# Kernel tuning notes

Measured on AMD Instinct MI355X. Metric: run time of the kernel, lower is better.

The kernel has to match this reference:

```python
import jax, jax.numpy as jnp
import numpy as np
import math

H, D = 8, 128            # num_heads, head_dim (hidden=1024)
CHUNK, PAST, FUT = 12, 12, 0
CTX = CHUNK + PAST + FUT  # 24
SOFTCAP = 50.0
INVALID = 1e-09
Q_SCALE = D ** (-0.5) / math.log(2)
K_SCALE = math.log(1.0 + math.e) / math.log(2)


def setup_inputs() -> dict:
    key = jax.random.key(0)
    ks = jax.random.split(key, 7)
    B, S, HS = 16, 2400, 1024
    w = lambda k: jax.random.normal(k, (HS, HS), jnp.float32) * 0.02
    return {
        "x": jax.random.normal(ks[0], (B, S, HS), jnp.float32),
        "pos_emb": jax.random.normal(ks[1], (CTX + 1, HS), jnp.float32),
        "Wq": w(ks[2]),
        "Wk": w(ks[3]),
        "Wv": w(ks[4]),
        "Wpost": w(ks[5]),
        "Wrel": w(ks[6]),
        "per_dim_scale": jnp.zeros((D,), jnp.float32),
    }


def _to_blocks(t):
    # [B,S,H,D] -> [B,nb,CHUNK,H,D] (pad S up to multiple of CHUNK)
    B, S, h, d = t.shape
    nb = -(-S // CHUNK)
    t = jnp.pad(t, ((0, 0), (0, nb * CHUNK - S), (0, 0), (0, 0)))
    return t.reshape(B, nb, CHUNK, h, d)


def _block_context(t):
    # [B,S,H,D] -> [B,nb,CTX,H,D]: per-block window of PAST left context + chunk + FUT
    B, S, h, d = t.shape
    nb = -(-S // CHUNK)
    tp = jnp.pad(t, ((0, 0), (PAST, FUT + CHUNK - 1), (0, 0), (0, 0)))
    idx = jnp.arange(nb)[:, None] * CHUNK + jnp.arange(CTX)[None, :]  # [nb,CTX]
    return tp[:, idx]  # gather -> [B,nb,CTX,H,D]


def _rel_shift(x):
    # [B,H,nb,CHUNK,P] -> [B,H,nb,CHUNK,CTX] via Transformer-XL reshape trick
    B, h, nb, bs, P = x.shape
    x = jnp.pad(x, ((0, 0), (0, 0), (0, 0), (0, 0), (0, CTX + 1 - P)))
    x = x.reshape(B, h, nb, bs * (CTX + 1))[..., : bs * CTX]
    return x.reshape(B, h, nb, bs, CTX)


def reference(x, pos_emb, Wq, Wk, Wv, Wpost, Wrel, per_dim_scale):
    B, S, HS = x.shape
    q = (x @ Wq).reshape(B, S, H, D) * Q_SCALE * jax.nn.softplus(per_dim_scale)
    k = (x @ Wk).reshape(B, S, H, D) * K_SCALE
    v = (x @ Wv).reshape(B, S, H, D)

    qb = _to_blocks(q)        # [B,nb,CHUNK,H,D]
    kc = _block_context(k)    # [B,nb,CTX,H,D]
    vc = _block_context(v)    # [B,nb,CTX,H,D]
    nb = qb.shape[1]

    rel_k = (pos_emb @ Wrel).reshape(-1, H, D)  # [P,H,D]

    # content-content scores: [B,H,nb,CHUNK,CTX]
    matrix_ac = jnp.einsum('bnqhd,bnkhd->bhnqk', qb, kc)
    # content-position scores with rel-shift: [B,H,nb,CHUNK,P] -> [...,CTX]
    matrix_bd = jnp.einsum('bnqhd,phd->bhnqp', qb, rel_k)
    matrix_bd = _rel_shift(matrix_bd)

    attn = jnp.tanh((matrix_ac + matrix_bd) / SOFTCAP) * SOFTCAP
    attn = jax.nn.softmax(attn, axis=-1)

    out = jnp.einsum('bhnqk,bnkhd->bnqhd', attn, vc)  # [B,nb,CHUNK,H,D]
    out = out.reshape(B, nb * CHUNK, H * D)[:, :S, :]
    return out @ Wpost
```

## Files before the change

### kernel.cpp

```cpp
#include <hip/hip_runtime.h>
#include <hip/hip_bf16.h>
#include <cmath>

#define AS_GLOBAL __attribute__((address_space(1)))
#define AS_LDS    __attribute__((address_space(3)))

typedef __attribute__((ext_vector_type(8))) short bf16x8;
typedef __attribute__((ext_vector_type(4))) float f32x4;
typedef unsigned short u16;

__device__ __forceinline__ u16 f2bf(float f) {
  union { __hip_bfloat16 h; u16 u; } cv;
  cv.h = __float2bfloat16(f);
  return cv.u;
}
__device__ __forceinline__ float bf2f(u16 u) {
  union { unsigned u32; float f; } v;
  v.u32 = ((unsigned)u) << 16;
  return v.f;
}


__global__ void k_f32_to_bf16(const float* __restrict__ in, u16* __restrict__ out, int n4) {
  int i = blockIdx.x * 256 + threadIdx.x;
  if (i >= n4) return;
  float4 v = ((const float4*)in)[i];
  ushort4 o;
  o.x = f2bf(v.x); o.y = f2bf(v.y); o.z = f2bf(v.z); o.w = f2bf(v.w);
  ((ushort4*)out)[i] = o;
}

__global__ void k_transpose_w(const float* __restrict__ in, u16* __restrict__ out) {
  __shared__ float tile[32][33];
  const int tx = threadIdx.x & 31;
  const int ty = threadIdx.x >> 5;
  const int x0 = blockIdx.x * 32, y0 = blockIdx.y * 32;
  #pragma unroll
  for (int i = 0; i < 32; i += 8)
    tile[ty + i][tx] = in[(size_t)(y0 + ty + i) * 1024 + x0 + tx];
  __syncthreads();
  #pragma unroll
  for (int i = 0; i < 32; i += 8)
    out[(size_t)(x0 + ty + i) * 1024 + y0 + tx] = f2bf(tile[tx][ty + i]);
}

__global__ void k_qscale(const float* __restrict__ pds, float* __restrict__ qs, float qscale_c) {
  int n = blockIdx.x * 256 + threadIdx.x;
  float s = pds[n & 127];
  qs[n] = qscale_c * log1pf(expf(s));
}

__global__ void k_relk(const float* __restrict__ pos, const u16* __restrict__ wrt,
                       u16* __restrict__ relkb) {
  __shared__ float prow[1024];
  const int tid = threadIdx.x;
  const int p = blockIdx.y;
  ((float4*)prow)[tid] = ((const float4*)(pos + (size_t)p * 1024))[tid];
  __syncthreads();
  int nn = blockIdx.x * 256 + tid;
  const u16* wr = wrt + (size_t)nn * 1024;
  float acc = 0.f;
  for (int kk = 0; kk < 1024; kk += 8) {
    ushort4 u0 = *(const ushort4*)(wr + kk);
    ushort4 u1 = *(const ushort4*)(wr + kk + 4);
    acc += bf2f(u0.x) * prow[kk + 0] + bf2f(u0.y) * prow[kk + 1]
         + bf2f(u0.z) * prow[kk + 2] + bf2f(u0.w) * prow[kk + 3]
         + bf2f(u1.x) * prow[kk + 4] + bf2f(u1.y) * prow[kk + 5]
         + bf2f(u1.z) * prow[kk + 6] + bf2f(u1.w) * prow[kk + 7];
  }
  relkb[(size_t)p * 1024 + nn] = f2bf(acc);
}


#define VMCNT(n) do { asm volatile("s_waitcnt vmcnt(" #n ")" ::: "memory"); \
                      __builtin_amdgcn_sched_barrier(0); } while (0)
#define BARF() do { asm volatile("" ::: "memory"); __builtin_amdgcn_s_barrier(); asm volatile("" ::: "memory"); } while (0)
#define GLD(SRC, DST) __builtin_amdgcn_global_load_lds((const AS_GLOBAL u16*)(SRC), (AS_LDS u16*)(DST), 16, 0, 0)
#define LDSA(d) ((AS_LDS char*)&lds[d][0][0])
#define LDSB(d) ((AS_LDS char*)&lds[d][1][0])

#define STAGE_A(d, h, t) do {                                                   \
  GLD(sA0 + (((size_t)(h)) << 6) * K + ((t) << 6), LDSA(d) + dA0 + ((h) << 13)); \
  GLD(sA1 + (((size_t)(h)) << 6) * K + ((t) << 6), LDSA(d) + dA1 + ((h) << 13)); \
} while (0)
#define STAGE_B(d, h, t) do {                                                   \
  GLD(sB0 + (((size_t)(h)) << 5) * K + ((t) << 6), LDSB(d) + dB0 + ((h) << 12)); \
  GLD(sB1 + (((size_t)(h)) << 5) * K + ((t) << 6), LDSB(d) + dB1 + ((h) << 12)); \
} while (0)

#define LOAD_A(d, qm) do {                                                       \
  _Pragma("unroll") for (int mi_ = 0; mi_ < 4; ++mi_) {                          \
    af[mi_][0] = *(const bf16x8*)&lds[d][0][abase + (((qm)*64 + mi_*16) << 6) + gk0]; \
    af[mi_][1] = *(const bf16x8*)&lds[d][0][abase + (((qm)*64 + mi_*16) << 6) + gk1]; \
  } } while (0)
#define LOAD_B(d, qn) do {                                                       \
  _Pragma("unroll") for (int ni_ = 0; ni_ < 2; ++ni_) {                          \
    bfb[ni_][0] = *(const bf16x8*)&lds[d][1][bbase + (((qn)*32 + ni_*16) << 6) + gk0]; \
    bfb[ni_][1] = *(const bf16x8*)&lds[d][1][bbase + (((qn)*32 + ni_*16) << 6) + gk1]; \
  } } while (0)
#define MFMA16(qm, qn) do {                                                      \
  __builtin_amdgcn_s_setprio(1);                                                 \
  _Pragma("unroll") for (int mi_ = 0; mi_ < 4; ++mi_)                            \
  _Pragma("unroll") for (int ni_ = 0; ni_ < 2; ++ni_) {                          \
    acc[(qm)*4+mi_][(qn)*2+ni_] = __builtin_amdgcn_mfma_f32_16x16x32_bf16(       \
        af[mi_][0], bfb[ni_][0], acc[(qm)*4+mi_][(qn)*2+ni_], 0, 0, 0);          \
    acc[(qm)*4+mi_][(qn)*2+ni_] = __builtin_amdgcn_mfma_f32_16x16x32_bf16(       \
        af[mi_][1], bfb[ni_][1], acc[(qm)*4+mi_][(qn)*2+ni_], 0, 0, 0);          \
  }                                                                              \
  __builtin_amdgcn_s_setprio(0); } while (0)

#define GEMM_MAINLOOP()                                                          \
  STAGE_B(0, 0, 0);  STAGE_A(0, 1, 0);  STAGE_A(0, 0, 0);  STAGE_B(0, 1, 0);     \
  STAGE_B(1, 0, 1);  STAGE_A(1, 1, 1);                                           \
  VMCNT(6);  BARF();                                                             \
  const int nk = K >> 6;                                                         \
  for (int i = 0; i < (nk >> 1) - 1; ++i) {                                      \
    const int t1 = 2 * i + 1, t2 = 2 * i + 2, t3 = 2 * i + 3;                    \
    LOAD_A(0, 0); LOAD_B(0, 0);                                                  \
    STAGE_A(1, 0, t1);                                                           \
    BARF(); MFMA16(0, 0); BARF();                                                \
    LOAD_A(0, 1);                                                                \
    STAGE_B(1, 1, t1);                                                           \
    BARF(); MFMA16(1, 0); VMCNT(8); BARF();                                      \
    LOAD_B(0, 1);                                                                \
    STAGE_B(0, 0, t2);                                                           \
    BARF(); MFMA16(1, 1); BARF();                                                \
    LOAD_A(0, 0);                                                                \
    STAGE_A(0, 1, t2);                                                           \
    BARF(); MFMA16(0, 1); VMCNT(6); BARF();                                      \
    LOAD_A(1, 0); LOAD_B(1, 0);                                                  \
    STAGE_A(0, 0, t2);                                                           \
    BARF(); MFMA16(0, 0); BARF();                                                \
    LOAD_A(1, 1);                                                                \
    STAGE_B(0, 1, t2);                                                           \
    BARF(); MFMA16(1, 0); VMCNT(8); BARF();                                      \
    LOAD_B(1, 1);                                                                \
    STAGE_B(1, 0, t3);                                                           \
    BARF(); MFMA16(1, 1); BARF();                                                \
    LOAD_A(1, 0);                                                                \
    STAGE_A(1, 1, t3);                                                           \
    BARF(); MFMA16(0, 1); VMCNT(6); BARF();                                      \
  }                                                                              \
  {                                                                              \
    const int t1 = nk - 1;                                                       \
    LOAD_A(0, 0); LOAD_B(0, 0);                                                  \
    STAGE_A(1, 0, t1);                                                           \
    BARF(); MFMA16(0, 0); BARF();                                                \
    LOAD_A(0, 1);                                                                \
    STAGE_B(1, 1, t1);                                                           \
    BARF(); MFMA16(1, 0); VMCNT(8); BARF();                                      \
    LOAD_B(0, 1);                                                                \
    BARF(); MFMA16(1, 1); BARF();                                                \
    LOAD_A(0, 0);                                                                \
    BARF(); MFMA16(0, 1); VMCNT(2); BARF();                                      \
    LOAD_A(1, 0); LOAD_B(1, 0);                                                  \
    BARF(); MFMA16(0, 0); BARF();                                                \
    LOAD_A(1, 1);                                                                \
    BARF(); MFMA16(1, 0); VMCNT(0); BARF();                                      \
    LOAD_B(1, 1);                                                                \
    BARF(); MFMA16(1, 1); BARF();                                                \
    LOAD_A(1, 0);                                                                \
    BARF(); MFMA16(0, 1);                                                        \
  }

#define GEMM_SETUP(NTN)                                                          \
  __shared__ __align__(16) u16 lds[2][2][16384];                                 \
  const int tid = threadIdx.x;                                                   \
  const int wave = tid >> 6, lane = tid & 63;                                    \
  const int l16 = lane & 15, quad = lane >> 4;                                   \
  const int wm = wave >> 2, wn = wave & 3;                                       \
  const int q8 = (int)gridDim.x >> 3;                                            \
  const int wg = ((int)blockIdx.x & 7) * q8 + ((int)blockIdx.x >> 3);            \
  const int m0 = (wg / (NTN)) << 8;                                              \
  const int n0 = (wg % (NTN)) << 8;                                              \
  const int sx = l16 & 7;                                                        \
  const int gk0 = (quad ^ sx) << 3;                                              \
  const int gk1 = ((4 + quad) ^ sx) << 3;                                        \
  const int abase = (wm * 128 + l16) << 6;                                       \
  const int bbase = (wn * 64 + l16) << 6;                                        \
  const int rl0 = tid >> 3, g0 = tid & 7;                                        \
  const int rl1 = rl0 + 64;                                                      \
  const int swz0 = (g0 ^ (rl0 & 7)) << 3;                                        \
  const int rbA0 = ((rl0 >> 6) << 7) + (rl0 & 63);                               \
  const int rbA1 = ((rl1 >> 6) << 7) + (rl1 & 63);                               \
  const int rbB0 = ((rl0 >> 5) << 6) + (rl0 & 31);                               \
  const int rbB1 = ((rl1 >> 5) << 6) + (rl1 & 31);                               \
  const u16* sA0 = A + (size_t)(m0 + rbA0) * K + swz0;                           \
  const u16* sA1 = A + (size_t)(m0 + rbA1) * K + swz0;                           \
  const u16* sB0 = Bt + (size_t)(n0 + rbB0) * K + swz0;                          \
  const u16* sB1 = Bt + (size_t)(n0 + rbB1) * K + swz0;                          \
  const int dA0 = (rbA0 << 7) + (g0 << 4);                                       \
  const int dA1 = (rbA1 << 7) + (g0 << 4);                                       \
  const int dB0 = (rbB0 << 7) + (g0 << 4);                                       \
  const int dB1 = (rbB1 << 7) + (g0 << 4);                                       \
  f32x4 acc[8][4];                                                               \
  _Pragma("unroll") for (int i = 0; i < 8; ++i)                                  \
    _Pragma("unroll") for (int j = 0; j < 4; ++j) {                              \
      f32x4 z = {0.f, 0.f, 0.f, 0.f};                                            \
      acc[i][j] = z;                                                             \
    }                                                                            \
  bf16x8 af[4][2], bfb[2][2];

__global__ __launch_bounds__(512, 2) void k_gemm256(
    const u16* __restrict__ A, const u16* __restrict__ Bt, float* __restrict__ Cout,
    int M, int N, int K) {
  GEMM_SETUP(N >> 8)
  GEMM_MAINLOOP()
  const int mb = m0 + wm * 128, nb = n0 + wn * 64;
  #pragma unroll
  for (int ni = 0; ni < 4; ++ni) {
    int col = nb + ni * 16 + l16;
    #pragma unroll
    for (int mi = 0; mi < 8; ++mi) {
      int row = mb + mi * 16 + quad * 4;
      #pragma unroll
      for (int r = 0; r < 4; ++r)
        Cout[(size_t)(row + r) * N + col] = acc[mi][ni][r];
    }
  }
}

__global__ __launch_bounds__(512, 2) void k_gemm_qkv(
    const u16* __restrict__ A, const u16* __restrict__ Bt,
    u16* __restrict__ Qo, u16* __restrict__ Ko, u16* __restrict__ Vt,
    const float* __restrict__ qsc, float ks, int M, int K) {
  GEMM_SETUP(12)
  GEMM_MAINLOOP()
  const int sec = n0 >> 10;
  const int mb = m0 + wm * 128;
  const int nbl = (n0 & 1023) + wn * 64;
  if (sec == 2) {
    #pragma unroll
    for (int ni = 0; ni < 4; ++ni) {
      int col = nbl + ni * 16 + l16;
      #pragma unroll
      for (int mi = 0; mi < 8; ++mi) {
        int row = mb + mi * 16 + quad * 4;
        ushort4 o;
        o.x = f2bf(acc[mi][ni][0]);
        o.y = f2bf(acc[mi][ni][1]);
        o.z = f2bf(acc[mi][ni][2]);
        o.w = f2bf(acc[mi][ni][3]);
        *(ushort4*)&Vt[(size_t)col * M + row] = o;
      }
    }
  } else {
    u16* Out = (sec == 0) ? Qo : Ko;
    #pragma unroll
    for (int ni = 0; ni < 4; ++ni) {
      int col = nbl + ni * 16 + l16;
      float cs = (sec == 0) ? qsc[col] : ks;
      #pragma unroll
      for (int mi = 0; mi < 8; ++mi) {
        int row = mb + mi * 16 + quad * 4;
        #pragma unroll
        for (int r = 0; r < 4; ++r)
          Out[(size_t)(row + r) * 1024 + col] = f2bf(acc[mi][ni][r] * cs);
      }
    }
  }
}

#undef GEMM_SETUP
#undef GEMM_MAINLOOP
#undef STAGE_A
#undef STAGE_B
#undef LOAD_A
#undef LOAD_B
#undef MFMA16

__global__ __launch_bounds__(256) void k_attn_mfma(
    const u16* __restrict__ q, const u16* __restrict__ k, const u16* __restrict__ vt,
    const u16* __restrict__ relkb, u16* __restrict__ ctx) {
  __shared__ float bdm_s[4][400];
  __shared__ u16 attnb[4][16 * 32];

  const int tid = threadIdx.x;
  const int w = tid >> 6, lane = tid & 63;
  const int l16 = lane & 15, quad = lane >> 4;

  for (int id0 = (int)blockIdx.x * 4; id0 < 25600; id0 += (int)gridDim.x * 4) {
    const int id = id0 + w;
    const int b = id / 1600;
    const int rr = id % 1600;
    const int n = rr >> 3, h = rr & 7;
    const int s0 = n * 12;
    const size_t rowbase = (size_t)b * 2400;

    bf16x8 qf[4];
    {
      int sq = s0 + l16;
      if (sq > 2399) sq = 2399;
      const u16* qp = q + ((rowbase + sq) * 1024 + (size_t)h * 128 + quad * 8);
      #pragma unroll
      for (int c = 0; c < 4; ++c) qf[c] = *(const bf16x8*)(qp + 32 * c);
    }

    #pragma unroll
    for (int pt = 0; pt < 2; ++pt) {
      int p = pt * 16 + l16;
      const u16* rp = relkb + ((size_t)p * 1024 + (size_t)h * 128 + quad * 8);
      f32x4 acc = {0.f, 0.f, 0.f, 0.f};
      #pragma unroll
      for (int c = 0; c < 4; ++c)
        acc = __builtin_amdgcn_mfma_f32_16x16x32_bf16(qf[c], *(const bf16x8*)(rp + 32 * c), acc, 0, 0, 0);
      if (p < 25) {
        #pragma unroll
        for (int r = 0; r < 4; ++r)
          bdm_s[w][(quad * 4 + r) * 25 + p] = acc[r];
      }
    }
    __threadfence_block();

    float l0[4], l1[4];
    #pragma unroll
    for (int kt = 0; kt < 2; ++kt) {
      int t = kt * 16 + l16;
      int sk = s0 - 12 + t;
      bool kvalid = ((unsigned)sk < 2400u);
      int ska = kvalid ? sk : 0;
      const u16* kp = k + ((rowbase + ska) * 1024 + (size_t)h * 128 + quad * 8);
      short km = kvalid ? (short)0xFFFF : (short)0;
      bf16x8 kmv = {km, km, km, km, km, km, km, km};
      f32x4 acc = {0.f, 0.f, 0.f, 0.f};
      #pragma unroll
      for (int c = 0; c < 4; ++c) {
        bf16x8 kf = *(const bf16x8*)(kp + 32 * c);
        kf &= kmv;
        acc = __builtin_amdgcn_mfma_f32_16x16x32_bf16(qf[c], kf, acc, 0, 0, 0);
      }
      #pragma unroll
      for (int r = 0; r < 4; ++r) {
        float bd = bdm_s[w][(quad * 4 + r) * 24 + t];
        float lg = tanhf((acc[r] + bd) * (1.0f / 50.0f)) * 50.0f;
        if (kt == 1 && l16 >= 8) lg = -INFINITY;
        if (kt) l1[r] = lg; else l0[r] = lg;
      }
    }

    float at0[4], at1[4];
    #pragma unroll
    for (int r = 0; r < 4; ++r) {
      float m = fmaxf(l0[r], l1[r]);
      #pragma unroll
      for (int s = 1; s < 16; s <<= 1) m = fmaxf(m, __shfl_xor(m, s, 64));
      float e0 = __expf(l0[r] - m), e1 = __expf(l1[r] - m);
      float sum = e0 + e1;
      #pragma unroll
      for (int s = 1; s < 16; s <<= 1) sum += __shfl_xor(sum, s, 64);
      float inv = 1.0f / sum;
      at0[r] = e0 * inv;
      at1[r] = e1 * inv;
    }

    #pragma unroll
    for (int r = 0; r < 4; ++r) {
      attnb[w][(quad * 4 + r) * 32 + l16] = f2bf(at0[r]);
      attnb[w][(quad * 4 + r) * 32 + 16 + l16] = f2bf(at1[r]);
    }
    __threadfence_block();
    bf16x8 paf = *(const bf16x8*)&attnb[w][l16 * 32 + quad * 8];

    int slo = s0 - 12 + quad * 8;
    bf16x8 vmsk;
    #pragma unroll
    for (int j = 0; j < 8; ++j)
      vmsk[j] = ((unsigned)(slo + j) < 2400u) ? (short)0xFFFF : (short)0;

    f32x4 oacc[8];
    #pragma unroll
    for (int dt = 0; dt < 8; ++dt) {
      int col = h * 128 + dt * 16 + l16;
      const u16* vp = vt + ((size_t)col * 38400 + (long)(rowbase + s0 - 12 + quad * 8));
      ushort4 va = *(const ushort4*)vp;
      ushort4 vb = *(const ushort4*)(vp + 4);
      bf16x8 vf = {(short)va.x, (short)va.y, (short)va.z, (short)va.w,
                   (short)vb.x, (short)vb.y, (short)vb.z, (short)vb.w};
      vf &= vmsk;
      f32x4 z = {0.f, 0.f, 0.f, 0.f};
      oacc[dt] = __builtin_amdgcn_mfma_f32_16x16x32_bf16(paf, vf, z, 0, 0, 0);
    }

    if (quad < 3) {
      #pragma unroll
      for (int dt = 0; dt < 8; ++dt) {
        int col = h * 128 + dt * 16 + l16;
        #pragma unroll
        for (int r = 0; r < 4; ++r) {
          int qi = quad * 4 + r;
          ctx[(rowbase + s0 + qi) * 1024 + col] = f2bf(oacc[dt][r]);
        }
      }
    }
  }
}


extern "C" void kernel_launch(void* const* d_in, const int* in_sizes, int n_in,
                              void* d_out, int out_size, void* d_ws, size_t ws_size,
                              hipStream_t stream) {
  const float* x       = (const float*)d_in[0];
  const float* pos_emb = (const float*)d_in[1];
  const float* Wq      = (const float*)d_in[2];
  const float* Wk      = (const float*)d_in[3];
  const float* Wv      = (const float*)d_in[4];
  const float* Wpost   = (const float*)d_in[5];
  const float* Wrel    = (const float*)d_in[6];
  const float* pds     = (const float*)d_in[7];
  float* out = (float*)d_out;

  const int M = 38400, HS = 1024;
  const size_t XE = (size_t)M * HS;

  u16* xbf = (u16*)d_ws;
  u16* qbf = xbf + XE;
  u16* kbf = qbf + XE;
  u16* vt_alloc = kbf + XE;
  u16* vt = vt_alloc + 16;
  u16* wqt = vt_alloc + XE + 64;
  u16* wkt = wqt + (size_t)HS * HS;
  u16* wvt = wkt + (size_t)HS * HS;
  u16* wrt = wvt + (size_t)HS * HS;
  u16* wpt = wrt + (size_t)HS * HS;
  u16* relkb = wpt + (size_t)HS * HS;
  float* qsc = (float*)(relkb + 32 * 1024);

  const double LN2 = 0.6931471805599453;
  const float QS = (float)((1.0 / sqrt(128.0)) / LN2);
  const float KS = (float)(log(1.0 + exp(1.0)) / LN2);

  k_f32_to_bf16<<<(int)(XE / 4 / 256), 256, 0, stream>>>(x, xbf, (int)(XE / 4));
  dim3 tg(32, 32);
  k_transpose_w<<<tg, 256, 0, stream>>>(Wq, wqt);
  k_transpose_w<<<tg, 256, 0, stream>>>(Wk, wkt);
  k_transpose_w<<<tg, 256, 0, stream>>>(Wv, wvt);
  k_transpose_w<<<tg, 256, 0, stream>>>(Wrel, wrt);
  k_transpose_w<<<tg, 256, 0, stream>>>(Wpost, wpt);
  k_qscale<<<4, 256, 0, stream>>>(pds, qsc, QS);
  k_relk<<<dim3(4, 25), 256, 0, stream>>>(pos_emb, wrt, relkb);
  k_gemm_qkv<<<(M / 256) * 12, 512, 0, stream>>>(xbf, wqt, qbf, kbf, vt, qsc, KS, M, HS);
  k_attn_mfma<<<2048, 256, 0, stream>>>(qbf, kbf, vt, relkb, xbf);
  k_gemm256<<<(M / 256) * (HS / 256), 512, 0, stream>>>(xbf, wpt, out, M, HS, HS);
}
```

Baseline: 798.3 us.

## Swap MFMA operands for row-contiguous vector stores and regroup QKV GEMM tile order

New measurement: 831.6 us. +4.2%, slower.

```diff
diff --git a/kernel.cpp b/kernel.cpp
--- a/kernel.cpp
+++ b/kernel.cpp
@@ -98,7 +98,7 @@
     bfb[ni_][0] = *(const bf16x8*)&lds[d][1][bbase + (((qn)*32 + ni_*16) << 6) + gk0]; \
     bfb[ni_][1] = *(const bf16x8*)&lds[d][1][bbase + (((qn)*32 + ni_*16) << 6) + gk1]; \
   } } while (0)
-#define MFMA16(qm, qn) do {                                                      \
+#define MFMA16_N(qm, qn) do {                                                    \
   __builtin_amdgcn_s_setprio(1);                                                 \
   _Pragma("unroll") for (int mi_ = 0; mi_ < 4; ++mi_)                            \
   _Pragma("unroll") for (int ni_ = 0; ni_ < 2; ++ni_) {                          \
@@ -108,8 +108,18 @@
         af[mi_][1], bfb[ni_][1], acc[(qm)*4+mi_][(qn)*2+ni_], 0, 0, 0);          \
   }                                                                              \
   __builtin_amdgcn_s_setprio(0); } while (0)
-
-#define GEMM_MAINLOOP()                                                          \
+#define MFMA16_S(qm, qn) do {                                                    \
+  __builtin_amdgcn_s_setprio(1);                                                 \
+  _Pragma("unroll") for (int mi_ = 0; mi_ < 4; ++mi_)                            \
+  _Pragma("unroll") for (int ni_ = 0; ni_ < 2; ++ni_) {                          \
+    acc[(qm)*4+mi_][(qn)*2+ni_] = __builtin_amdgcn_mfma_f32_16x16x32_bf16(       \
+        bfb[ni_][0], af[mi_][0], acc[(qm)*4+mi_][(qn)*2+ni_], 0, 0, 0);          \
+    acc[(qm)*4+mi_][(qn)*2+ni_] = __builtin_amdgcn_mfma_f32_16x16x32_bf16(       \
+        bfb[ni_][1], af[mi_][1], acc[(qm)*4+mi_][(qn)*2+ni_], 0, 0, 0);          \
+  }                                                                              \
+  __builtin_amdgcn_s_setprio(0); } while (0)
+
+#define GEMM_MAINLOOP(MM)                                                        \
   STAGE_B(0, 0, 0);  STAGE_A(0, 1, 0);  STAGE_A(0, 0, 0);  STAGE_B(0, 1, 0);     \
   STAGE_B(1, 0, 1);  STAGE_A(1, 1, 1);                                           \
   VMCNT(6);  BARF();                                                             \
@@ -118,61 +128,52 @@
     const int t1 = 2 * i + 1, t2 = 2 * i + 2, t3 = 2 * i + 3;                    \
     LOAD_A(0, 0); LOAD_B(0, 0);                                                  \
     STAGE_A(1, 0, t1);                                                           \
-    BARF(); MFMA16(0, 0); BARF();                                                \
+    BARF(); MM(0, 0); BARF();                                                    \
     LOAD_A(0, 1);                                                                \
     STAGE_B(1, 1, t1);                                                           \
-    BARF(); MFMA16(1, 0); VMCNT(8); BARF();                                      \
+    BARF(); MM(1, 0); VMCNT(8); BARF();                                          \
     LOAD_B(0, 1);                                                                \
     STAGE_B(0, 0, t2);                                                           \
-    BARF(); MFMA16(1, 1); BARF();                                                \
+    BARF(); MM(1, 1); BARF();                                                    \
     LOAD_A(0, 0);                                                                \
     STAGE_A(0, 1, t2);                                                           \
-    BARF(); MFMA16(0, 1); VMCNT(6); BARF();                                      \
+    BARF(); MM(0, 1); VMCNT(6); BARF();                                          \
     LOAD_A(1, 0); LOAD_B(1, 0);                                                  \
     STAGE_A(0, 0, t2);                                                           \
-    BARF(); MFMA16(0, 0); BARF();                                                \
+    BARF(); MM(0, 0); BARF();                                                    \
     LOAD_A(1, 1);                                                                \
     STAGE_B(0, 1, t2);                                                           \
-    BARF(); MFMA16(1, 0); VMCNT(8); BARF();                                      \
+    BARF(); MM(1, 0); VMCNT(8); BARF();                                          \
     LOAD_B(1, 1);                                                                \
     STAGE_B(1, 0, t3);                                                           \
-    BARF(); MFMA16(1, 1); BARF();                                                \
+    BARF(); MM(1, 1); BARF();                                                    \
     LOAD_A(1, 0);                                                                \
     STAGE_A(1, 1, t3);                                                           \
-    BARF(); MFMA16(0, 1); VMCNT(6); BARF();                                      \
+    BARF(); MM(0, 1); VMCNT(6); BARF();                                          \
   }                                                                              \
   {                                                                              \
     const int t1 = nk - 1;                                                       \
     LOAD_A(0, 0); LOAD_B(0, 0);                                                  \
     STAGE_A(1, 0, t1);                                                           \
-    BARF(); MFMA16(0, 0); BARF();                                                \
+    BARF(); MM(0, 0); BARF();                                                    \
     LOAD_A(0, 1);                                                                \
     STAGE_B(1, 1, t1);                                                           \
-    BARF(); MFMA16(1, 0); VMCNT(8); BARF();                                      \
+    BARF(); MM(1, 0); VMCNT(8); BARF();                                          \
     LOAD_B(0, 1);                                                                \
-    BARF(); MFMA16(1, 1); BARF();                                                \
+    BARF(); MM(1, 1); BARF();                                                    \
     LOAD_A(0, 0);                                                                \
-    BARF(); MFMA16(0, 1); VMCNT(2); BARF();                                      \
+    BARF(); MM(0, 1); VMCNT(2); BARF();                                          \
     LOAD_A(1, 0); LOAD_B(1, 0);                                                  \
-    BARF(); MFMA16(0, 0); BARF();                                                \
+    BARF(); MM(0, 0); BARF();                                                    \
     LOAD_A(1, 1);                                                                \
-    BARF(); MFMA16(1, 0); VMCNT(0); BARF();                                      \
+    BARF(); MM(1, 0); VMCNT(0); BARF();                                          \
     LOAD_B(1, 1);                                                                \
-    BARF(); MFMA16(1, 1); BARF();                                                \
+    BARF(); MM(1, 1); BARF();                                                    \
     LOAD_A(1, 0);                                                                \
-    BARF(); MFMA16(0, 1);                                                        \
+    BARF(); MM(0, 1);                                                            \
   }
 
-#define GEMM_SETUP(NTN)                                                          \
-  __shared__ __align__(16) u16 lds[2][2][16384];                                 \
-  const int tid = threadIdx.x;                                                   \
-  const int wave = tid >> 6, lane = tid & 63;                                    \
-  const int l16 = lane & 15, quad = lane >> 4;                                   \
-  const int wm = wave >> 2, wn = wave & 3;                                       \
-  const int q8 = (int)gridDim.x >> 3;                                            \
-  const int wg = ((int)blockIdx.x & 7) * q8 + ((int)blockIdx.x >> 3);            \
-  const int m0 = (wg / (NTN)) << 8;                                              \
-  const int n0 = (wg % (NTN)) << 8;                                              \
+#define GEMM_SETUP()                                                             \
   const int sx = l16 & 7;                                                        \
   const int gk0 = (quad ^ sx) << 3;                                              \
   const int gk1 = ((4 + quad) ^ sx) << 3;                                        \
@@ -204,18 +205,26 @@
 __global__ __launch_bounds__(512, 2) void k_gemm256(
     const u16* __restrict__ A, const u16* __restrict__ Bt, float* __restrict__ Cout,
     int M, int N, int K) {
-  GEMM_SETUP(N >> 8)
-  GEMM_MAINLOOP()
+  __shared__ __align__(16) u16 lds[2][2][16384];
+  const int tid = threadIdx.x;
+  const int wave = tid >> 6, lane = tid & 63;
+  const int l16 = lane & 15, quad = lane >> 4;
+  const int wm = wave >> 2, wn = wave & 3;
+  const int q8 = (int)gridDim.x >> 3;
+  const int wg = ((int)blockIdx.x & 7) * q8 + ((int)blockIdx.x >> 3);
+  const int ntn = N >> 8;
+  const int m0 = (wg / ntn) << 8;
+  const int n0 = (wg % ntn) << 8;
+  GEMM_SETUP()
+  GEMM_MAINLOOP(MFMA16_S)
   const int mb = m0 + wm * 128, nb = n0 + wn * 64;
   #pragma unroll
   for (int ni = 0; ni < 4; ++ni) {
-    int col = nb + ni * 16 + l16;
+    int colb = nb + ni * 16 + quad * 4;
     #pragma unroll
     for (int mi = 0; mi < 8; ++mi) {
-      int row = mb + mi * 16 + quad * 4;
-      #pragma unroll
-      for (int r = 0; r < 4; ++r)
-        Cout[(size_t)(row + r) * N + col] = acc[mi][ni][r];
+      int row = mb + mi * 16 + l16;
+      *(f32x4*)&Cout[(size_t)row * N + colb] = acc[mi][ni];
     }
   }
 }
@@ -224,12 +233,22 @@
     const u16* __restrict__ A, const u16* __restrict__ Bt,
     u16* __restrict__ Qo, u16* __restrict__ Ko, u16* __restrict__ Vt,
     const float* __restrict__ qsc, float ks, int M, int K) {
-  GEMM_SETUP(12)
-  GEMM_MAINLOOP()
+  __shared__ __align__(16) u16 lds[2][2][16384];
+  const int tid = threadIdx.x;
+  const int wave = tid >> 6, lane = tid & 63;
+  const int l16 = lane & 15, quad = lane >> 4;
+  const int wm = wave >> 2, wn = wave & 3;
+  const int q8 = (int)gridDim.x >> 3;
+  const int wg = ((int)blockIdx.x & 7) * q8 + ((int)blockIdx.x >> 3);
+  const int sg = wg / 9, lcl = wg % 9;
+  const int m0 = ((sg >> 2) * 3 + lcl / 3) << 8;
+  const int n0 = ((sg & 3) * 3 + lcl % 3) << 8;
+  GEMM_SETUP()
   const int sec = n0 >> 10;
   const int mb = m0 + wm * 128;
   const int nbl = (n0 & 1023) + wn * 64;
   if (sec == 2) {
+    GEMM_MAINLOOP(MFMA16_N)
     #pragma unroll
     for (int ni = 0; ni < 4; ++ni) {
       int col = nbl + ni * 16 + l16;
@@ -245,17 +264,23 @@
       }
     }
   } else {
+    GEMM_MAINLOOP(MFMA16_S)
     u16* Out = (sec == 0) ? Qo : Ko;
     #pragma unroll
     for (int ni = 0; ni < 4; ++ni) {
-      int col = nbl + ni * 16 + l16;
-      float cs = (sec == 0) ? qsc[col] : ks;
+      int colb = nbl + ni * 16 + quad * 4;
+      float4 sc;
+      if (sec == 0) sc = *(const float4*)&qsc[colb];
+      else { sc.x = ks; sc.y = ks; sc.z = ks; sc.w = ks; }
       #pragma unroll
       for (int mi = 0; mi < 8; ++mi) {
-        int row = mb + mi * 16 + quad * 4;
-        #pragma unroll
-        for (int r = 0; r < 4; ++r)
-          Out[(size_t)(row + r) * 1024 + col] = f2bf(acc[mi][ni][r] * cs);
+        int row = mb + mi * 16 + l16;
+        ushort4 o;
+        o.x = f2bf(acc[mi][ni][0] * sc.x);
+        o.y = f2bf(acc[mi][ni][1] * sc.y);
+        o.z = f2bf(acc[mi][ni][2] * sc.z);
+        o.w = f2bf(acc[mi][ni][3] * sc.w);
+        *(ushort4*)&Out[(size_t)row * 1024 + colb] = o;
       }
     }
   }
@@ -267,7 +292,8 @@
 #undef STAGE_B
 #undef LOAD_A
 #undef LOAD_B
-#undef MFMA16
+#undef MFMA16_N
+#undef MFMA16_S
 
 __global__ __launch_bounds__(256) void k_attn_mfma(
     const u16* __restrict__ q, const u16* __restrict__ k, const u16* __restrict__ vt,
@@ -439,6 +465,6 @@
   k_qscale<<<4, 256, 0, stream>>>(pds, qsc, QS);
   k_relk<<<dim3(4, 25), 256, 0, stream>>>(pos_emb, wrt, relkb);
   k_gemm_qkv<<<(M / 256) * 12, 512, 0, stream>>>(xbf, wqt, qbf, kbf, vt, qsc, KS, M, HS);
-  k_attn_mfma<<<2048, 256, 0, stream>>>(qbf, kbf, vt, relkb, xbf);
+  k_attn_mfma<<<1600, 256, 0, stream>>>(qbf, kbf, vt, relkb, xbf);
   k_gemm256<<<(M / 256) * (HS / 256), 512, 0, stream>>>(xbf, wpt, out, M, HS, HS);
 }
```

## Restructure GEMM main loop pipeline with full two-stage prefetch and B-fragment reuse

Applied to the files above, without the earlier changes.

Result: no change. 802.9 us (+0.6%).

```diff
diff --git a/kernel.cpp b/kernel.cpp
--- a/kernel.cpp
+++ b/kernel.cpp
@@ -95,72 +95,67 @@
   } } while (0)
 #define LOAD_B(d, qn) do {                                                       \
   _Pragma("unroll") for (int ni_ = 0; ni_ < 2; ++ni_) {                          \
-    bfb[ni_][0] = *(const bf16x8*)&lds[d][1][bbase + (((qn)*32 + ni_*16) << 6) + gk0]; \
-    bfb[ni_][1] = *(const bf16x8*)&lds[d][1][bbase + (((qn)*32 + ni_*16) << 6) + gk1]; \
+    bfb[(qn)*2+ni_][0] = *(const bf16x8*)&lds[d][1][bbase + (((qn)*32 + ni_*16) << 6) + gk0]; \
+    bfb[(qn)*2+ni_][1] = *(const bf16x8*)&lds[d][1][bbase + (((qn)*32 + ni_*16) << 6) + gk1]; \
   } } while (0)
 #define MFMA16(qm, qn) do {                                                      \
   __builtin_amdgcn_s_setprio(1);                                                 \
   _Pragma("unroll") for (int mi_ = 0; mi_ < 4; ++mi_)                            \
   _Pragma("unroll") for (int ni_ = 0; ni_ < 2; ++ni_) {                          \
     acc[(qm)*4+mi_][(qn)*2+ni_] = __builtin_amdgcn_mfma_f32_16x16x32_bf16(       \
-        af[mi_][0], bfb[ni_][0], acc[(qm)*4+mi_][(qn)*2+ni_], 0, 0, 0);          \
+        af[mi_][0], bfb[(qn)*2+ni_][0], acc[(qm)*4+mi_][(qn)*2+ni_], 0, 0, 0);   \
     acc[(qm)*4+mi_][(qn)*2+ni_] = __builtin_amdgcn_mfma_f32_16x16x32_bf16(       \
-        af[mi_][1], bfb[ni_][1], acc[(qm)*4+mi_][(qn)*2+ni_], 0, 0, 0);          \
+        af[mi_][1], bfb[(qn)*2+ni_][1], acc[(qm)*4+mi_][(qn)*2+ni_], 0, 0, 0);   \
   }                                                                              \
   __builtin_amdgcn_s_setprio(0); } while (0)
 
 #define GEMM_MAINLOOP()                                                          \
-  STAGE_B(0, 0, 0);  STAGE_A(0, 1, 0);  STAGE_A(0, 0, 0);  STAGE_B(0, 1, 0);     \
-  STAGE_B(1, 0, 1);  STAGE_A(1, 1, 1);                                           \
-  VMCNT(6);  BARF();                                                             \
+  STAGE_A(0, 0, 0); STAGE_B(0, 0, 0); STAGE_B(0, 1, 0); STAGE_A(0, 1, 0);        \
+  STAGE_A(1, 0, 1); STAGE_B(1, 0, 1); STAGE_B(1, 1, 1); STAGE_A(1, 1, 1);        \
+  VMCNT(12);  BARF();                                                            \
   const int nk = K >> 6;                                                         \
   for (int i = 0; i < (nk >> 1) - 1; ++i) {                                      \
-    const int t1 = 2 * i + 1, t2 = 2 * i + 2, t3 = 2 * i + 3;                    \
+    const int t2 = 2 * i + 2, t3 = 2 * i + 3;                                    \
+                                                     \
     LOAD_A(0, 0); LOAD_B(0, 0);                                                  \
-    STAGE_A(1, 0, t1);                                                           \
-    BARF(); MFMA16(0, 0); BARF();                                                \
+    BARF(); MFMA16(0, 0); VMCNT(10); BARF();                                     \
+                             \
+    LOAD_B(0, 1);                                                                \
+    STAGE_A(0, 0, t2); STAGE_B(0, 0, t2);                                        \
+    BARF(); MFMA16(0, 1); VMCNT(12); BARF();                                     \
+                                \
     LOAD_A(0, 1);                                                                \
-    STAGE_B(1, 1, t1);                                                           \
-    BARF(); MFMA16(1, 0); VMCNT(8); BARF();                                      \
-    LOAD_B(0, 1);                                                                \
-    STAGE_B(0, 0, t2);                                                           \
-    BARF(); MFMA16(1, 1); BARF();                                                \
-    LOAD_A(0, 0);                                                                \
+    STAGE_B(0, 1, t2);                                                           \
+    BARF(); MFMA16(1, 0); BARF();                                                \
+                                         \
     STAGE_A(0, 1, t2);                                                           \
-    BARF(); MFMA16(0, 1); VMCNT(6); BARF();                                      \
+    BARF(); MFMA16(1, 1); VMCNT(12); BARF();                                     \
+                                                     \
     LOAD_A(1, 0); LOAD_B(1, 0);                                                  \
-    STAGE_A(0, 0, t2);                                                           \
-    BARF(); MFMA16(0, 0); BARF();                                                \
+    BARF(); MFMA16(0, 0); VMCNT(10); BARF();                                     \
+    LOAD_B(1, 1);                                                                \
+    STAGE_A(1, 0, t3); STAGE_B(1, 0, t3);                                        \
+    BARF(); MFMA16(0, 1); VMCNT(12); BARF();                                     \
     LOAD_A(1, 1);                                                                \
-    STAGE_B(0, 1, t2);                                                           \
-    BARF(); MFMA16(1, 0); VMCNT(8); BARF();                                      \
-    LOAD_B(1, 1);                                                                \
-    STAGE_B(1, 0, t3);                                                           \
-    BARF(); MFMA16(1, 1); BARF();                                                \
-    LOAD_A(1, 0);                                                                \
+    STAGE_B(1, 1, t3);                                                           \
+    BARF(); MFMA16(1, 0); BARF();                                                \
     STAGE_A(1, 1, t3);                                                           \
-    BARF(); MFMA16(0, 1); VMCNT(6); BARF();                                      \
+    BARF(); MFMA16(1, 1); VMCNT(12); BARF();                                     \
   }                                                                              \
   {                                                                              \
-    const int t1 = nk - 1;                                                       \
+        \
     LOAD_A(0, 0); LOAD_B(0, 0);                                                  \
-    STAGE_A(1, 0, t1);                                                           \
-    BARF(); MFMA16(0, 0); BARF();                                                \
+    BARF(); MFMA16(0, 0); VMCNT(10); BARF();                                     \
+    LOAD_B(0, 1);                                                                \
+    BARF(); MFMA16(0, 1); VMCNT(8); BARF();                                      \
     LOAD_A(0, 1);                                                                \
-    STAGE_B(1, 1, t1);                                                           \
-    BARF(); MFMA16(1, 0); VMCNT(8); BARF();                                      \
-    LOAD_B(0, 1);                                                                \
-    BARF(); MFMA16(1, 1); BARF();                                                \
-    LOAD_A(0, 0);                                                                \
-    BARF(); MFMA16(0, 1); VMCNT(2); BARF();                                      \
+    BARF(); MFMA16(1, 0); MFMA16(1, 1); VMCNT(4); BARF();                        \
     LOAD_A(1, 0); LOAD_B(1, 0);                                                  \
-    BARF(); MFMA16(0, 0); BARF();                                                \
+    BARF(); MFMA16(0, 0); VMCNT(2); BARF();                                      \
+    LOAD_B(1, 1);                                                                \
+    BARF(); MFMA16(0, 1); VMCNT(0); BARF();                                      \
     LOAD_A(1, 1);                                                                \
-    BARF(); MFMA16(1, 0); VMCNT(0); BARF();                                      \
-    LOAD_B(1, 1);                                                                \
-    BARF(); MFMA16(1, 1); BARF();                                                \
-    LOAD_A(1, 0);                                                                \
-    BARF(); MFMA16(0, 1);                                                        \
+    BARF(); MFMA16(1, 0); MFMA16(1, 1);                                          \
   }
 
 #define GEMM_SETUP(NTN)                                                          \
@@ -199,7 +194,7 @@
       f32x4 z = {0.f, 0.f, 0.f, 0.f};                                            \
       acc[i][j] = z;                                                             \
     }                                                                            \
-  bf16x8 af[4][2], bfb[2][2];
+  bf16x8 af[4][2], bfb[4][2];
 
 __global__ __launch_bounds__(512, 2) void k_gemm256(
     const u16* __restrict__ A, const u16* __restrict__ Bt, float* __restrict__ Cout,
```
